# Performance work log

Hardware: AMD Instinct MI355X
Metric: run time of the kernel (lower is better)

The kernel has to match this reference:

```python
import jax, jax.numpy as jnp
import numpy as np

B, IN, E, H, V, MAX_LEN = 512, 64, 512, 1024, 1024, 32
LN_EPS = 1e-5


def setup_inputs() -> dict:
    key = jax.random.key(0)
    ks = jax.random.split(key, 16)
    s = 0.02
    n = lambda k, shp: jax.random.normal(k, shp, jnp.float32) * s
    return {
        "x": jax.random.normal(ks[0], (B, IN), jnp.float32),
        "w_in": n(ks[1], (E, IN)), "b_in": jnp.zeros((E,), jnp.float32),
        "w_ih0": n(ks[2], (4 * H, E)), "w_hh0": n(ks[3], (4 * H, H)),
        "b_ih0": jnp.zeros((4 * H,), jnp.float32), "b_hh0": jnp.zeros((4 * H,), jnp.float32),
        "w_ih1": n(ks[4], (4 * H, H)), "w_hh1": n(ks[5], (4 * H, H)),
        "b_ih1": jnp.zeros((4 * H,), jnp.float32), "b_hh1": jnp.zeros((4 * H,), jnp.float32),
        "ln_g": jnp.ones((H,), jnp.float32), "ln_b": jnp.zeros((H,), jnp.float32),
        "w_out": n(ks[6], (V, H)), "b_out": jnp.zeros((V,), jnp.float32),
        "emb": n(ks[7], (V, E)),
    }


def _lstm_cell(x, h, c, w_ih, w_hh, b_ih, b_hh):
    # PyTorch LSTMCell: gates ordered (input, forget, cell, output)
    gates = x @ w_ih.T + h @ w_hh.T + b_ih + b_hh  # [B, 4H]
    i, f, g, o = jnp.split(gates, 4, axis=1)
    i, f, o = jax.nn.sigmoid(i), jax.nn.sigmoid(f), jax.nn.sigmoid(o)
    g = jnp.tanh(g)
    c2 = f * c + i * g
    h2 = o * jnp.tanh(c2)
    return h2, c2


def reference(x, w_in, b_in, w_ih0, w_hh0, b_ih0, b_hh0,
              w_ih1, w_hh1, b_ih1, b_hh1, ln_g, ln_b, w_out, b_out, emb):
    bsz = x.shape[0]
    hid = w_hh0.shape[1]
    inp = x @ w_in.T + b_in  # [B, E]
    z = jnp.zeros((bsz, hid), jnp.float32)
    init = (z, z, z, z, inp)

    def step(carry, _):
        h0, c0, h1, c1, cur = carry
        h0, c0 = _lstm_cell(cur, h0, c0, w_ih0, w_hh0, b_ih0, b_hh0)
        h1, c1 = _lstm_cell(h0, h1, c1, w_ih1, w_hh1, b_ih1, b_hh1)
        mu = jnp.mean(h1, axis=-1, keepdims=True)
        var = jnp.mean((h1 - mu) ** 2, axis=-1, keepdims=True)
        hn = (h1 - mu) / jnp.sqrt(var + LN_EPS) * ln_g + ln_b
        lp = jax.nn.log_softmax(hn @ w_out.T + b_out, axis=-1)  # [B, V]
        ent = -jnp.sum(jnp.exp(lp) * lp, axis=-1)  # [B]
        sym = jnp.argmax(lp, axis=-1)  # eval-mode (deterministic) path
        logprob = jnp.take_along_axis(lp, sym[:, None], axis=1)[:, 0]
        nxt = emb[sym]  # [B, E]
        return (h0, c0, h1, c1, nxt), (sym, logprob, ent)

    _, (seq, logits, ent) = jax.lax.scan(step, init, None, length=MAX_LEN)
    seq, logits, ent = seq.T, logits.T, ent.T  # [B, MAX_LEN]
    zcol_f = jnp.zeros((bsz, 1), jnp.float32)
    zcol_i = jnp.zeros((bsz, 1), seq.dtype)
    seq = jnp.concatenate([seq, zcol_i], axis=1)
    logits = jnp.concatenate([logits, zcol_f], axis=1)
    ent = jnp.concatenate([ent, zcol_f], axis=1)
    return seq, logits, ent
```

## Files before the change

### kernel.cpp

```cpp
#include <hip/hip_runtime.h>
#include <hip/hip_bf16.h>
#include <math.h>

#define BQ   512
#define EDIM 512
#define HDIM 1024
#define VDIM 1024
#define TLEN 32
#define TOUT 33
#define PGS  (BQ * 4 * HDIM)
#define PLS  (BQ * VDIM)

typedef _Float16 half8  __attribute__((ext_vector_type(8)));
typedef _Float16 half4v __attribute__((ext_vector_type(4)));
typedef float    f32x16 __attribute__((ext_vector_type(16)));

#define GLOAD_LDS16(gp, lp) __builtin_amdgcn_global_load_lds( \
    (const __attribute__((address_space(1))) void*)(gp),      \
    (__attribute__((address_space(3))) void*)(lp), 16, 0, 0)

__device__ __forceinline__ size_t packoff(int r, int k, int K) {
    return (size_t)(r >> 5) * (size_t)(32 * K) + (size_t)(k >> 4) * 512
         + (size_t)((k >> 3) & 1) * 256 + (size_t)(r & 31) * 8 + (size_t)(k & 7);
}

__device__ _Float16 g_curh[BQ*EDIM], g_curl[BQ*EDIM];
__device__ _Float16 g_h0h[BQ*HDIM], g_h0l[BQ*HDIM];
__device__ _Float16 g_h1h[BQ*HDIM], g_h1l[BQ*HDIM];
__device__ _Float16 g_hnh[BQ*HDIM], g_hnl[BQ*HDIM];
__device__ float    g_c0[BQ*HDIM], g_c1[BQ*HDIM];

__device__ _Float16 g_wih0h[4*HDIM*EDIM], g_wih0l[4*HDIM*EDIM];
__device__ _Float16 g_whh0h[4*HDIM*HDIM], g_whh0l[4*HDIM*HDIM];
__device__ _Float16 g_wih1h[4*HDIM*HDIM], g_wih1l[4*HDIM*HDIM];
__device__ _Float16 g_whh1h[4*HDIM*HDIM], g_whh1l[4*HDIM*HDIM];
__device__ _Float16 g_wouth[VDIM*HDIM],   g_woutl[VDIM*HDIM];

__device__ float g_part_g[4 * PGS];
__device__ float g_part_lg[8 * PLS];
__device__ float g_bsum0[4*HDIM], g_bsum1[4*HDIM];

__global__ void init_kernel(float* __restrict__ out,
                            const float* __restrict__ bi0, const float* __restrict__ bh0,
                            const float* __restrict__ bi1, const float* __restrict__ bh1) {
    int i = blockIdx.x * 256 + threadIdx.x;
    g_c0[i] = 0.f; g_c1[i] = 0.f;
    g_h0h[i] = (_Float16)0.f; g_h0l[i] = (_Float16)0.f;
    g_h1h[i] = (_Float16)0.f; g_h1l[i] = (_Float16)0.f;
    if (i < 4 * HDIM) {
        g_bsum0[i] = bi0[i] + bh0[i];
        g_bsum1[i] = bi1[i] + bh1[i];
    }
    if (i < 3 * BQ) {
        int which = i / BQ, b = i % BQ;
        out[(size_t)which * BQ * TOUT + (size_t)b * TOUT + (TOUT - 1)] = 0.f;
    }
}

__global__ void split_pack_kernel(const float* __restrict__ w, _Float16* __restrict__ hi,
                                  _Float16* __restrict__ lo, int klog, int nquads) {
    int q = blockIdx.x * 256 + threadIdx.x;
    if (q >= nquads) return;
    int e = q * 4;
    int r = e >> klog, k = e & ((1 << klog) - 1);
    float4 v = ((const float4*)w)[q];
    half4v h, l;
    h[0] = (_Float16)v.x; l[0] = (_Float16)((v.x - (float)h[0]) * 4096.f);
    h[1] = (_Float16)v.y; l[1] = (_Float16)((v.y - (float)h[1]) * 4096.f);
    h[2] = (_Float16)v.z; l[2] = (_Float16)((v.z - (float)h[2]) * 4096.f);
    h[3] = (_Float16)v.w; l[3] = (_Float16)((v.w - (float)h[3]) * 4096.f);
    size_t po = packoff(r, k, 1 << klog);
    *(half4v*)&hi[po] = h;
    *(half4v*)&lo[po] = l;
}

__device__ __forceinline__ void split1(float x, _Float16* hp, _Float16* lp) {
    _Float16 h = (_Float16)x;
    *hp = h;
    *lp = (_Float16)((x - (float)h) * 4096.f);
}

__global__ __launch_bounds__(256, 2) void gemm_rb(
    const _Float16* __restrict__ Ah1, const _Float16* __restrict__ Al1, int K1,
    const _Float16* __restrict__ Wh1, const _Float16* __restrict__ Wl1,
    const _Float16* __restrict__ Ah2, const _Float16* __restrict__ Al2, int K2,
    const _Float16* __restrict__ Wh2, const _Float16* __restrict__ Wl2,
    float* __restrict__ outp, int N, int S, int NTP)
{
    __shared__ __align__(16) _Float16 sA[4][2][4][512];
    __shared__ __align__(16) _Float16 sB[4][2][4][512];
    int tid = threadIdx.x;
    int l = tid & 63, w = tid >> 6;
    int lr = l & 31, lq = l >> 5;
    int mw = w >> 1, nw = w & 1;

    int wb = blockIdx.x;
    int xcd = wb & 7, q = wb >> 3;
    int nt = xcd * NTP + q % NTP;
    int rest = q / NTP;
    int s = rest % S;
    int mb = rest / S;

    int kch1 = K1 / S, kch2 = (K2 > 0) ? (K2 / S) : 0;
    int n1 = kch1 >> 4;
    int nit = n1 + (kch2 >> 4);

    const _Float16* fsrc1[4];
    const _Float16* fsrc2[4];
    _Float16* fdst0[4];
    #pragma unroll
    for (int qq = 0; qq < 4; ++qq) {
        int fq = w * 4 + qq;
        bool isA = fq < 8;
        int r_ = isA ? fq : fq - 8;
        int pl = r_ >> 2, idx = r_ & 3;
        int strip = isA ? (mb * 4 + idx) : (nt * 4 + idx);
        const _Float16* p1 = isA ? (pl ? Al1 : Ah1) : (pl ? Wl1 : Wh1);
        fsrc1[qq] = p1 + (size_t)strip * (size_t)(32 * K1)
                  + (size_t)((s * kch1) >> 4) * 512 + (size_t)l * 8;
        if (K2 > 0) {
            const _Float16* p2 = isA ? (pl ? Al2 : Ah2) : (pl ? Wl2 : Wh2);
            fsrc2[qq] = p2 + (size_t)strip * (size_t)(32 * K2)
                      + (size_t)((s * kch2) >> 4) * 512 + (size_t)l * 8;
        } else {
            fsrc2[qq] = fsrc1[qq];
        }
        fdst0[qq] = isA ? &sA[0][pl][idx][0] : &sB[0][pl][idx][0];
    }

    f32x16 accM00 = {}, accM01 = {}, accM10 = {}, accM11 = {};
    f32x16 accL00 = {}, accL01 = {}, accL10 = {}, accL11 = {};

#define STAGE(IT, SLOT)                                                        \
    {                                                                          \
        int it_ = (IT);                                                        \
        bool g1_ = it_ < n1;                                                   \
        size_t off_ = (size_t)(g1_ ? it_ : it_ - n1) * 512;                    \
        _Pragma("unroll")                                                      \
        for (int qq = 0; qq < 4; ++qq) {                                       \
            const _Float16* sp_ = (g1_ ? fsrc1[qq] : fsrc2[qq]) + off_;        \
            GLOAD_LDS16(sp_, fdst0[qq] + (size_t)(SLOT) * 4096);               \
        }                                                                      \
    }

#define COMPUTE(BUF)                                                           \
    {                                                                          \
        half8 ah0 = *(const half8*)&sA[BUF][0][2*mw  ][(size_t)l * 8];         \
        half8 ah1 = *(const half8*)&sA[BUF][0][2*mw+1][(size_t)l * 8];         \
        half8 al0 = *(const half8*)&sA[BUF][1][2*mw  ][(size_t)l * 8];         \
        half8 al1 = *(const half8*)&sA[BUF][1][2*mw+1][(size_t)l * 8];         \
        half8 bh0 = *(const half8*)&sB[BUF][0][2*nw  ][(size_t)l * 8];         \
        half8 bh1 = *(const half8*)&sB[BUF][0][2*nw+1][(size_t)l * 8];         \
        half8 bl0 = *(const half8*)&sB[BUF][1][2*nw  ][(size_t)l * 8];         \
        half8 bl1 = *(const half8*)&sB[BUF][1][2*nw+1][(size_t)l * 8];         \
        accM00 = __builtin_amdgcn_mfma_f32_32x32x16_f16(ah0, bh0, accM00, 0, 0, 0); \
        accM01 = __builtin_amdgcn_mfma_f32_32x32x16_f16(ah0, bh1, accM01, 0, 0, 0); \
        accM10 = __builtin_amdgcn_mfma_f32_32x32x16_f16(ah1, bh0, accM10, 0, 0, 0); \
        accM11 = __builtin_amdgcn_mfma_f32_32x32x16_f16(ah1, bh1, accM11, 0, 0, 0); \
        accL00 = __builtin_amdgcn_mfma_f32_32x32x16_f16(ah0, bl0, accL00, 0, 0, 0); \
        accL01 = __builtin_amdgcn_mfma_f32_32x32x16_f16(ah0, bl1, accL01, 0, 0, 0); \
        accL10 = __builtin_amdgcn_mfma_f32_32x32x16_f16(ah1, bl0, accL10, 0, 0, 0); \
        accL11 = __builtin_amdgcn_mfma_f32_32x32x16_f16(ah1, bl1, accL11, 0, 0, 0); \
        accL00 = __builtin_amdgcn_mfma_f32_32x32x16_f16(al0, bh0, accL00, 0, 0, 0); \
        accL01 = __builtin_amdgcn_mfma_f32_32x32x16_f16(al0, bh1, accL01, 0, 0, 0); \
        accL10 = __builtin_amdgcn_mfma_f32_32x32x16_f16(al1, bh0, accL10, 0, 0, 0); \
        accL11 = __builtin_amdgcn_mfma_f32_32x32x16_f16(al1, bh1, accL11, 0, 0, 0); \
    }

#define WAITSYNC(IT)                                                           \
    {                                                                          \
        if ((IT) < nit - 2)       asm volatile("s_waitcnt vmcnt(8)" ::: "memory"); \
        else if ((IT) == nit - 2) asm volatile("s_waitcnt vmcnt(4)" ::: "memory"); \
        else                      asm volatile("s_waitcnt vmcnt(0)" ::: "memory"); \
        __builtin_amdgcn_sched_barrier(0);                                     \
        __builtin_amdgcn_s_barrier();                                          \
    }

    STAGE(0, 0);
    STAGE(1, 1);
    for (int it = 0; it < nit; ++it) {
        if (it + 2 < nit) STAGE(it + 2, (it + 2) & 3);
        WAITSYNC(it);
        COMPUTE(it & 3);
    }
#undef WAITSYNC
#undef COMPUTE
#undef STAGE

    float* op = outp + (size_t)s * BQ * N;
    #pragma unroll
    for (int mi = 0; mi < 2; ++mi) {
        int m0 = mb * 128 + (mw * 2 + mi) * 32;
        #pragma unroll
        for (int ni = 0; ni < 2; ++ni) {
            int n = nt * 128 + (nw * 2 + ni) * 32 + lr;
            const f32x16* aM = (mi == 0) ? (ni == 0 ? &accM00 : &accM01)
                                         : (ni == 0 ? &accM10 : &accM11);
            const f32x16* aL = (mi == 0) ? (ni == 0 ? &accL00 : &accL01)
                                         : (ni == 0 ? &accL10 : &accL11);
            #pragma unroll
            for (int r = 0; r < 16; ++r) {
                int row = (r & 3) + 8 * (r >> 2) + 4 * lq;
                op[(size_t)(m0 + row) * N + n] = (*aM)[r] + (*aL)[r] * (1.f / 4096.f);
            }
        }
    }
}

#define GBK 16
#define GPAD 68
__global__ __launch_bounds__(256) void gemm_in(const float* __restrict__ x,
                                               const float* __restrict__ w_in,
                                               const float* __restrict__ b_in) {
    __shared__ __align__(16) float As[GBK][GPAD];
    __shared__ __align__(16) float Bs[GBK][GPAD];
    int tid = threadIdx.x;
    int tx = tid & 15, ty = tid >> 4;
    int m0 = blockIdx.y * 64, n0 = blockIdx.x * 64;
    int lm = tid >> 2, lk = (tid & 3) << 2;
    const int K = 64;
    float acc[4][4] = {};
    for (int k0 = 0; k0 < K; k0 += GBK) {
        float4 av = *(const float4*)(x + (size_t)(m0 + lm) * K + k0 + lk);
        float4 wv = *(const float4*)(w_in + (size_t)(n0 + lm) * K + k0 + lk);
        As[lk + 0][lm] = av.x; As[lk + 1][lm] = av.y;
        As[lk + 2][lm] = av.z; As[lk + 3][lm] = av.w;
        Bs[lk + 0][lm] = wv.x; Bs[lk + 1][lm] = wv.y;
        Bs[lk + 2][lm] = wv.z; Bs[lk + 3][lm] = wv.w;
        __syncthreads();
        #pragma unroll
        for (int kk = 0; kk < GBK; ++kk) {
            float4 a  = *(const float4*)&As[kk][ty * 4];
            float4 bq = *(const float4*)&Bs[kk][tx * 4];
            float aa[4] = {a.x, a.y, a.z, a.w};
            float bb[4] = {bq.x, bq.y, bq.z, bq.w};
            #pragma unroll
            for (int i = 0; i < 4; ++i)
                #pragma unroll
                for (int j = 0; j < 4; ++j)
                    acc[i][j] = fmaf(aa[i], bb[j], acc[i][j]);
        }
        __syncthreads();
    }
    #pragma unroll
    for (int i = 0; i < 4; ++i) {
        int m = m0 + ty * 4 + i;
        int n = n0 + tx * 4;
        half4v h, lo;
        #pragma unroll
        for (int j = 0; j < 4; ++j) {
            float v = acc[i][j] + b_in[n + j];
            _Float16 hv = (_Float16)v;
            h[j] = hv;
            lo[j] = (_Float16)((v - (float)hv) * 4096.f);
        }
        size_t po = packoff(m, n, EDIM);
        *(half4v*)&g_curh[po] = h;
        *(half4v*)&g_curl[po] = lo;
    }
}

__device__ __forceinline__ float sigm(float x) { return 1.f / (1.f + expf(-x)); }

__global__ void lstm0_kernel() {
    int qidx = blockIdx.x * 256 + threadIdx.x;
    int b = qidx >> 8;
    int j = (qidx & 255) * 4;
    size_t base = (size_t)b * 4096;
    float4 G[4];
    #pragma unroll
    for (int g = 0; g < 4; ++g) {
        float4 bs = *(const float4*)&g_bsum0[g * 1024 + j];
        G[g] = bs;
        #pragma unroll
        for (int s = 0; s < 4; ++s) {
            float4 p = *(const float4*)&g_part_g[(size_t)s * PGS + base + g * 1024 + j];
            G[g].x += p.x; G[g].y += p.y; G[g].z += p.z; G[g].w += p.w;
        }
    }
    size_t hb = (size_t)b * HDIM + j;
    float4 cin = *(const float4*)&g_c0[hb];
    float ci[4] = {cin.x, cin.y, cin.z, cin.w};
    float gi[4] = {G[0].x, G[0].y, G[0].z, G[0].w};
    float gf[4] = {G[1].x, G[1].y, G[1].z, G[1].w};
    float gg[4] = {G[2].x, G[2].y, G[2].z, G[2].w};
    float go[4] = {G[3].x, G[3].y, G[3].z, G[3].w};
    float c[4], h[4];
    half4v hh, hl;
    #pragma unroll
    for (int r = 0; r < 4; ++r) {
        c[r] = sigm(gf[r]) * ci[r] + sigm(gi[r]) * tanhf(gg[r]);
        h[r] = sigm(go[r]) * tanhf(c[r]);
        _Float16 hi16 = (_Float16)h[r];
        hh[r] = hi16;
        hl[r] = (_Float16)((h[r] - (float)hi16) * 4096.f);
    }
    *(float4*)&g_c0[hb] = {c[0], c[1], c[2], c[3]};
    size_t po = packoff(b, j, HDIM);
    *(half4v*)&g_h0h[po] = hh;
    *(half4v*)&g_h0l[po] = hl;
}

__global__ __launch_bounds__(256) void lstm1_ln_kernel(
    const float* __restrict__ ln_g, const float* __restrict__ ln_b)
{
    __shared__ float sbuf[4];
    int b = blockIdx.x, tid = threadIdx.x;
    int lane = tid & 63, wid = tid >> 6;
    int j = tid * 4;
    size_t base = (size_t)b * 4096;
    float4 G[4];
    #pragma unroll
    for (int g = 0; g < 4; ++g) {
        float4 bs = *(const float4*)&g_bsum1[g * 1024 + j];
        G[g] = bs;
        #pragma unroll
        for (int s = 0; s < 4; ++s) {
            float4 p = *(const float4*)&g_part_g[(size_t)s * PGS + base + g * 1024 + j];
            G[g].x += p.x; G[g].y += p.y; G[g].z += p.z; G[g].w += p.w;
        }
    }
    size_t hb = (size_t)b * HDIM + j;
    float4 cin = *(const float4*)&g_c1[hb];
    float ci[4] = {cin.x, cin.y, cin.z, cin.w};
    float gi[4] = {G[0].x, G[0].y, G[0].z, G[0].w};
    float gf[4] = {G[1].x, G[1].y, G[1].z, G[1].w};
    float gg[4] = {G[2].x, G[2].y, G[2].z, G[2].w};
    float go[4] = {G[3].x, G[3].y, G[3].z, G[3].w};
    float c[4], h[4];
    float sum = 0.f;
    #pragma unroll
    for (int r = 0; r < 4; ++r) {
        c[r] = sigm(gf[r]) * ci[r] + sigm(gi[r]) * tanhf(gg[r]);
        h[r] = sigm(go[r]) * tanhf(c[r]);
        sum += h[r];
    }
    *(float4*)&g_c1[hb] = {c[0], c[1], c[2], c[3]};
    size_t po = packoff(b, j, HDIM);
    half4v h1h, h1l;
    #pragma unroll
    for (int r = 0; r < 4; ++r) {
        _Float16 hi16 = (_Float16)h[r];
        h1h[r] = hi16;
        h1l[r] = (_Float16)((h[r] - (float)hi16) * 4096.f);
    }
    *(half4v*)&g_h1h[po] = h1h;
    *(half4v*)&g_h1l[po] = h1l;

    for (int off = 32; off > 0; off >>= 1) sum += __shfl_down(sum, off, 64);
    if (lane == 0) sbuf[wid] = sum;
    __syncthreads();
    float mu = (sbuf[0] + sbuf[1] + sbuf[2] + sbuf[3]) * (1.f / HDIM);
    __syncthreads();
    float sq = 0.f;
    #pragma unroll
    for (int r = 0; r < 4; ++r) { float d = h[r] - mu; sq += d * d; }
    for (int off = 32; off > 0; off >>= 1) sq += __shfl_down(sq, off, 64);
    if (lane == 0) sbuf[wid] = sq;
    __syncthreads();
    float var = (sbuf[0] + sbuf[1] + sbuf[2] + sbuf[3]) * (1.f / HDIM);
    float rstd = 1.f / sqrtf(var + 1e-5f);
    half4v nh, nl;
    #pragma unroll
    for (int r = 0; r < 4; ++r) {
        float hn = (h[r] - mu) * rstd * ln_g[j + r] + ln_b[j + r];
        _Float16 hi16 = (_Float16)hn;
        nh[r] = hi16;
        nl[r] = (_Float16)((hn - (float)hi16) * 4096.f);
    }
    *(half4v*)&g_hnh[po] = nh;
    *(half4v*)&g_hnl[po] = nl;
}

__global__ __launch_bounds__(256) void softmax_row_kernel(
    const float* __restrict__ b_out, const float* __restrict__ emb,
    float* __restrict__ out, int t)
{
    __shared__ float swv[4];
    __shared__ int   swi[4];
    __shared__ float sZ[4], sS[4];
    __shared__ float s_max;
    __shared__ int   s_idx;
    int b = blockIdx.x, tid = threadIdx.x;
    int lane = tid & 63, wid = tid >> 6;
    size_t base = (size_t)b * VDIM + 4 * tid;
    float4 xv = *(const float4*)&b_out[4 * tid];
    #pragma unroll
    for (int s = 0; s < 8; ++s) {
        float4 p = *(const float4*)&g_part_lg[(size_t)s * PLS + base];
        xv.x += p.x; xv.y += p.y; xv.z += p.z; xv.w += p.w;
    }

    float mv = xv.x; int mi = 4 * tid;
    if (xv.y > mv) { mv = xv.y; mi = 4 * tid + 1; }
    if (xv.z > mv) { mv = xv.z; mi = 4 * tid + 2; }
    if (xv.w > mv) { mv = xv.w; mi = 4 * tid + 3; }
    for (int off = 32; off > 0; off >>= 1) {
        float ov = __shfl_down(mv, off, 64);
        int   oi = __shfl_down(mi, off, 64);
        if (ov > mv || (ov == mv && oi < mi)) { mv = ov; mi = oi; }
    }
    if (lane == 0) { swv[wid] = mv; swi[wid] = mi; }
    __syncthreads();
    if (tid == 0) {
        mv = swv[0]; mi = swi[0];
        for (int w = 1; w < 4; ++w)
            if (swv[w] > mv || (swv[w] == mv && swi[w] < mi)) { mv = swv[w]; mi = swi[w]; }
        s_max = mv; s_idx = mi;
    }
    __syncthreads();
    float xmax = s_max;

    float sv[4] = {xv.x - xmax, xv.y - xmax, xv.z - xmax, xv.w - xmax};
    float z = 0.f, s1 = 0.f;
    #pragma unroll
    for (int r = 0; r < 4; ++r) { float e = expf(sv[r]); z += e; s1 += e * sv[r]; }
    for (int off = 32; off > 0; off >>= 1) {
        z  += __shfl_down(z, off, 64);
        s1 += __shfl_down(s1, off, 64);
    }
    if (lane == 0) { sZ[wid] = z; sS[wid] = s1; }
    __syncthreads();
    if (tid == 0) {
        float Z = sZ[0] + sZ[1] + sZ[2] + sZ[3];
        float S1 = sS[0] + sS[1] + sS[2] + sS[3];
        float logZ = logf(Z);
        float ent = logZ - S1 / Z;
        out[(size_t)b * TOUT + t]                         = (float)s_idx;
        out[(size_t)BQ * TOUT + (size_t)b * TOUT + t]     = -logZ;
        out[(size_t)2 * BQ * TOUT + (size_t)b * TOUT + t] = ent;
    }
    __syncthreads();
    int sym = s_idx;
    const float* e = emb + (size_t)sym * EDIM;
    for (int j = tid; j < EDIM; j += 256) {
        size_t po = packoff(b, j, EDIM);
        split1(e[j], &g_curh[po], &g_curl[po]);
    }
}

extern "C" void kernel_launch(void* const* d_in, const int* in_sizes, int n_in,
                              void* d_out, int out_size, void* d_ws, size_t ws_size,
                              hipStream_t stream) {
    const float* x     = (const float*)d_in[0];
    const float* w_in  = (const float*)d_in[1];
    const float* b_in  = (const float*)d_in[2];
    const float* w_ih0 = (const float*)d_in[3];
    const float* w_hh0 = (const float*)d_in[4];
    const float* b_ih0 = (const float*)d_in[5];
    const float* b_hh0 = (const float*)d_in[6];
    const float* w_ih1 = (const float*)d_in[7];
    const float* w_hh1 = (const float*)d_in[8];
    const float* b_ih1 = (const float*)d_in[9];
    const float* b_hh1 = (const float*)d_in[10];
    const float* ln_g  = (const float*)d_in[11];
    const float* ln_b  = (const float*)d_in[12];
    const float* w_out = (const float*)d_in[13];
    const float* b_out = (const float*)d_in[14];
    const float* emb   = (const float*)d_in[15];
    float* out = (float*)d_out;

    _Float16 *wih0h, *wih0l, *whh0h, *whh0l, *wih1h, *wih1l, *whh1h, *whh1l, *wouth, *woutl;
    hipGetSymbolAddress((void**)&wih0h, HIP_SYMBOL(g_wih0h));
    hipGetSymbolAddress((void**)&wih0l, HIP_SYMBOL(g_wih0l));
    hipGetSymbolAddress((void**)&whh0h, HIP_SYMBOL(g_whh0h));
    hipGetSymbolAddress((void**)&whh0l, HIP_SYMBOL(g_whh0l));
    hipGetSymbolAddress((void**)&wih1h, HIP_SYMBOL(g_wih1h));
    hipGetSymbolAddress((void**)&wih1l, HIP_SYMBOL(g_wih1l));
    hipGetSymbolAddress((void**)&whh1h, HIP_SYMBOL(g_whh1h));
    hipGetSymbolAddress((void**)&whh1l, HIP_SYMBOL(g_whh1l));
    hipGetSymbolAddress((void**)&wouth, HIP_SYMBOL(g_wouth));
    hipGetSymbolAddress((void**)&woutl, HIP_SYMBOL(g_woutl));
    _Float16 *curh, *curl, *h0h, *h0l, *h1h, *h1l, *hnh, *hnl;
    hipGetSymbolAddress((void**)&curh, HIP_SYMBOL(g_curh));
    hipGetSymbolAddress((void**)&curl, HIP_SYMBOL(g_curl));
    hipGetSymbolAddress((void**)&h0h, HIP_SYMBOL(g_h0h));
    hipGetSymbolAddress((void**)&h0l, HIP_SYMBOL(g_h0l));
    hipGetSymbolAddress((void**)&h1h, HIP_SYMBOL(g_h1h));
    hipGetSymbolAddress((void**)&h1l, HIP_SYMBOL(g_h1l));
    hipGetSymbolAddress((void**)&hnh, HIP_SYMBOL(g_hnh));
    hipGetSymbolAddress((void**)&hnl, HIP_SYMBOL(g_hnl));
    float *part_g, *part_lg;
    hipGetSymbolAddress((void**)&part_g, HIP_SYMBOL(g_part_g));
    hipGetSymbolAddress((void**)&part_lg, HIP_SYMBOL(g_part_lg));

    init_kernel<<<(BQ * HDIM) / 256, 256, 0, stream>>>(out, b_ih0, b_hh0, b_ih1, b_hh1);

    split_pack_kernel<<<(4*HDIM*EDIM/4 + 255)/256, 256, 0, stream>>>(w_ih0, wih0h, wih0l, 9,  4*HDIM*EDIM/4);
    split_pack_kernel<<<(4*HDIM*HDIM/4 + 255)/256, 256, 0, stream>>>(w_hh0, whh0h, whh0l, 10, 4*HDIM*HDIM/4);
    split_pack_kernel<<<(4*HDIM*HDIM/4 + 255)/256, 256, 0, stream>>>(w_ih1, wih1h, wih1l, 10, 4*HDIM*HDIM/4);
    split_pack_kernel<<<(4*HDIM*HDIM/4 + 255)/256, 256, 0, stream>>>(w_hh1, whh1h, whh1l, 10, 4*HDIM*HDIM/4);
    split_pack_kernel<<<(VDIM*HDIM/4 + 255)/256, 256, 0, stream>>>(w_out, wouth, woutl, 10, VDIM*HDIM/4);

    gemm_in<<<dim3(EDIM / 64, BQ / 64), 256, 0, stream>>>(x, w_in, b_in);

    for (int t = 0; t < TLEN; ++t) {
        gemm_rb<<<512, 256, 0, stream>>>(
            curh, curl, EDIM, wih0h, wih0l,
            h0h, h0l, HDIM, whh0h, whh0l,
            part_g, 4 * HDIM, 4, 4);
        lstm0_kernel<<<(BQ * HDIM / 4) / 256, 256, 0, stream>>>();

        gemm_rb<<<512, 256, 0, stream>>>(
            h0h, h0l, HDIM, wih1h, wih1l,
            h1h, h1l, HDIM, whh1h, whh1l,
            part_g, 4 * HDIM, 4, 4);
        lstm1_ln_kernel<<<BQ, 256, 0, stream>>>(ln_g, ln_b);

        gemm_rb<<<256, 256, 0, stream>>>(
            hnh, hnl, HDIM, wouth, woutl,
            (const _Float16*)nullptr, (const _Float16*)nullptr, 0,
            (const _Float16*)nullptr, (const _Float16*)nullptr,
            part_lg, VDIM, 8, 1);

        softmax_row_kernel<<<BQ, 256, 0, stream>>>(b_out, emb, out, t);
    }
}
```

Before: 2.968 ms.

## Load B weight fragments directly into registers instead of staging through LDS

The GEMM now stages only the A operand through shared memory with global_load_lds and loads each wave's B (weight) fragments straight from global memory into registers, double-buffered across two register sets with the loop unrolled by two. The aim is to halve LDS traffic and footprint, since each B fragment is used by only one wave pair. It also wraps the MFMA chain in s_setprio. The vmcnt accounting is adjusted, but the loop assumes an even iteration count and adds register pressure, with possible uncoalesced or exposed global latency on B.

```diff
diff --git a/kernel.cpp b/kernel.cpp
--- a/kernel.cpp
+++ b/kernel.cpp
@@ -88,7 +88,6 @@
     float* __restrict__ outp, int N, int S, int NTP)
 {
     __shared__ __align__(16) _Float16 sA[4][2][4][512];
-    __shared__ __align__(16) _Float16 sB[4][2][4][512];
     int tid = threadIdx.x;
     int l = tid & 63, w = tid >> 6;
     int lr = l & 31, lq = l >> 5;
@@ -105,87 +104,122 @@
     int n1 = kch1 >> 4;
     int nit = n1 + (kch2 >> 4);
 
-    const _Float16* fsrc1[4];
-    const _Float16* fsrc2[4];
-    _Float16* fdst0[4];
-    #pragma unroll
-    for (int qq = 0; qq < 4; ++qq) {
-        int fq = w * 4 + qq;
-        bool isA = fq < 8;
-        int r_ = isA ? fq : fq - 8;
-        int pl = r_ >> 2, idx = r_ & 3;
-        int strip = isA ? (mb * 4 + idx) : (nt * 4 + idx);
-        const _Float16* p1 = isA ? (pl ? Al1 : Ah1) : (pl ? Wl1 : Wh1);
-        fsrc1[qq] = p1 + (size_t)strip * (size_t)(32 * K1)
-                  + (size_t)((s * kch1) >> 4) * 512 + (size_t)l * 8;
+    const _Float16* fsrcA1[2];
+    const _Float16* fsrcA2[2];
+    _Float16* fdstA[2];
+    #pragma unroll
+    for (int qq = 0; qq < 2; ++qq) {
+        int f = w * 2 + qq;
+        int pl = f >> 2, mf = f & 3;
+        const _Float16* p1 = pl ? Al1 : Ah1;
+        fsrcA1[qq] = p1 + (size_t)(mb * 4 + mf) * (size_t)(32 * K1)
+                   + (size_t)((s * kch1) >> 4) * 512 + (size_t)l * 8;
         if (K2 > 0) {
-            const _Float16* p2 = isA ? (pl ? Al2 : Ah2) : (pl ? Wl2 : Wh2);
-            fsrc2[qq] = p2 + (size_t)strip * (size_t)(32 * K2)
-                      + (size_t)((s * kch2) >> 4) * 512 + (size_t)l * 8;
+            const _Float16* p2 = pl ? Al2 : Ah2;
+            fsrcA2[qq] = p2 + (size_t)(mb * 4 + mf) * (size_t)(32 * K2)
+                       + (size_t)((s * kch2) >> 4) * 512 + (size_t)l * 8;
         } else {
-            fsrc2[qq] = fsrc1[qq];
-        }
-        fdst0[qq] = isA ? &sA[0][pl][idx][0] : &sB[0][pl][idx][0];
+            fsrcA2[qq] = fsrcA1[qq];
+        }
+        fdstA[qq] = &sA[0][pl][mf][0];
+    }
+
+    const _Float16 *pB1[4], *pB2[4];
+    #pragma unroll
+    for (int pj = 0; pj < 4; ++pj) {
+        int pl = pj >> 1, j = pj & 1;
+        const _Float16* p1 = pl ? Wl1 : Wh1;
+        pB1[pj] = p1 + (size_t)(nt * 4 + 2 * nw + j) * (size_t)(32 * K1)
+                + (size_t)((s * kch1) >> 4) * 512 + (size_t)l * 8;
+        if (K2 > 0) {
+            const _Float16* p2 = pl ? Wl2 : Wh2;
+            pB2[pj] = p2 + (size_t)(nt * 4 + 2 * nw + j) * (size_t)(32 * K2)
+                    + (size_t)((s * kch2) >> 4) * 512 + (size_t)l * 8;
+        } else {
+            pB2[pj] = pB1[pj];
+        }
     }
 
     f32x16 accM00 = {}, accM01 = {}, accM10 = {}, accM11 = {};
     f32x16 accL00 = {}, accL01 = {}, accL10 = {}, accL11 = {};
 
-#define STAGE(IT, SLOT)                                                        \
+    half8 B0h0, B0h1, B0l0, B0l1;
+    half8 B1h0, B1h1, B1l0, B1l1;
+
+#define STAGE_A(IT, SLOT)                                                      \
     {                                                                          \
         int it_ = (IT);                                                        \
         bool g1_ = it_ < n1;                                                   \
         size_t off_ = (size_t)(g1_ ? it_ : it_ - n1) * 512;                    \
         _Pragma("unroll")                                                      \
-        for (int qq = 0; qq < 4; ++qq) {                                       \
-            const _Float16* sp_ = (g1_ ? fsrc1[qq] : fsrc2[qq]) + off_;        \
-            GLOAD_LDS16(sp_, fdst0[qq] + (size_t)(SLOT) * 4096);               \
+        for (int qq = 0; qq < 2; ++qq) {                                       \
+            const _Float16* sp_ = (g1_ ? fsrcA1[qq] : fsrcA2[qq]) + off_;      \
+            GLOAD_LDS16(sp_, fdstA[qq] + (size_t)(SLOT) * 4096);               \
         }                                                                      \
     }
 
-#define COMPUTE(BUF)                                                           \
+#define LOAD_B(IT, BH0, BH1, BL0, BL1)                                         \
     {                                                                          \
-        half8 ah0 = *(const half8*)&sA[BUF][0][2*mw  ][(size_t)l * 8];         \
-        half8 ah1 = *(const half8*)&sA[BUF][0][2*mw+1][(size_t)l * 8];         \
-        half8 al0 = *(const half8*)&sA[BUF][1][2*mw  ][(size_t)l * 8];         \
-        half8 al1 = *(const half8*)&sA[BUF][1][2*mw+1][(size_t)l * 8];         \
-        half8 bh0 = *(const half8*)&sB[BUF][0][2*nw  ][(size_t)l * 8];         \
-        half8 bh1 = *(const half8*)&sB[BUF][0][2*nw+1][(size_t)l * 8];         \
-        half8 bl0 = *(const half8*)&sB[BUF][1][2*nw  ][(size_t)l * 8];         \
-        half8 bl1 = *(const half8*)&sB[BUF][1][2*nw+1][(size_t)l * 8];         \
-        accM00 = __builtin_amdgcn_mfma_f32_32x32x16_f16(ah0, bh0, accM00, 0, 0, 0); \
-        accM01 = __builtin_amdgcn_mfma_f32_32x32x16_f16(ah0, bh1, accM01, 0, 0, 0); \
-        accM10 = __builtin_amdgcn_mfma_f32_32x32x16_f16(ah1, bh0, accM10, 0, 0, 0); \
-        accM11 = __builtin_amdgcn_mfma_f32_32x32x16_f16(ah1, bh1, accM11, 0, 0, 0); \
-        accL00 = __builtin_amdgcn_mfma_f32_32x32x16_f16(ah0, bl0, accL00, 0, 0, 0); \
-        accL01 = __builtin_amdgcn_mfma_f32_32x32x16_f16(ah0, bl1, accL01, 0, 0, 0); \
-        accL10 = __builtin_amdgcn_mfma_f32_32x32x16_f16(ah1, bl0, accL10, 0, 0, 0); \
-        accL11 = __builtin_amdgcn_mfma_f32_32x32x16_f16(ah1, bl1, accL11, 0, 0, 0); \
-        accL00 = __builtin_amdgcn_mfma_f32_32x32x16_f16(al0, bh0, accL00, 0, 0, 0); \
-        accL01 = __builtin_amdgcn_mfma_f32_32x32x16_f16(al0, bh1, accL01, 0, 0, 0); \
-        accL10 = __builtin_amdgcn_mfma_f32_32x32x16_f16(al1, bh0, accL10, 0, 0, 0); \
-        accL11 = __builtin_amdgcn_mfma_f32_32x32x16_f16(al1, bh1, accL11, 0, 0, 0); \
+        int it_ = (IT);                                                        \
+        bool g1_ = it_ < n1;                                                   \
+        size_t off_ = (size_t)(g1_ ? it_ : it_ - n1) * 512;                    \
+        BH0 = *(const half8*)((g1_ ? pB1[0] : pB2[0]) + off_);                 \
+        BH1 = *(const half8*)((g1_ ? pB1[1] : pB2[1]) + off_);                 \
+        BL0 = *(const half8*)((g1_ ? pB1[2] : pB2[2]) + off_);                 \
+        BL1 = *(const half8*)((g1_ ? pB1[3] : pB2[3]) + off_);                 \
+    }
+
+#define COMPUTE(SLOT, BH0, BH1, BL0, BL1)                                      \
+    {                                                                          \
+        half8 ah0 = *(const half8*)&sA[SLOT][0][2*mw  ][(size_t)l * 8];        \
+        half8 ah1 = *(const half8*)&sA[SLOT][0][2*mw+1][(size_t)l * 8];        \
+        half8 al0 = *(const half8*)&sA[SLOT][1][2*mw  ][(size_t)l * 8];        \
+        half8 al1 = *(const half8*)&sA[SLOT][1][2*mw+1][(size_t)l * 8];        \
+        __builtin_amdgcn_s_setprio(1);                                         \
+        accM00 = __builtin_amdgcn_mfma_f32_32x32x16_f16(ah0, BH0, accM00, 0, 0, 0); \
+        accM01 = __builtin_amdgcn_mfma_f32_32x32x16_f16(ah0, BH1, accM01, 0, 0, 0); \
+        accM10 = __builtin_amdgcn_mfma_f32_32x32x16_f16(ah1, BH0, accM10, 0, 0, 0); \
+        accM11 = __builtin_amdgcn_mfma_f32_32x32x16_f16(ah1, BH1, accM11, 0, 0, 0); \
+        accL00 = __builtin_amdgcn_mfma_f32_32x32x16_f16(ah0, BL0, accL00, 0, 0, 0); \
+        accL01 = __builtin_amdgcn_mfma_f32_32x32x16_f16(ah0, BL1, accL01, 0, 0, 0); \
+        accL10 = __builtin_amdgcn_mfma_f32_32x32x16_f16(ah1, BL0, accL10, 0, 0, 0); \
+        accL11 = __builtin_amdgcn_mfma_f32_32x32x16_f16(ah1, BL1, accL11, 0, 0, 0); \
+        accL00 = __builtin_amdgcn_mfma_f32_32x32x16_f16(al0, BH0, accL00, 0, 0, 0); \
+        accL01 = __builtin_amdgcn_mfma_f32_32x32x16_f16(al0, BH1, accL01, 0, 0, 0); \
+        accL10 = __builtin_amdgcn_mfma_f32_32x32x16_f16(al1, BH0, accL10, 0, 0, 0); \
+        accL11 = __builtin_amdgcn_mfma_f32_32x32x16_f16(al1, BH1, accL11, 0, 0, 0); \
+        __builtin_amdgcn_s_setprio(0);                                         \
     }
 
 #define WAITSYNC(IT)                                                           \
     {                                                                          \
-        if ((IT) < nit - 2)       asm volatile("s_waitcnt vmcnt(8)" ::: "memory"); \
-        else if ((IT) == nit - 2) asm volatile("s_waitcnt vmcnt(4)" ::: "memory"); \
-        else                      asm volatile("s_waitcnt vmcnt(0)" ::: "memory"); \
+        int rem_ = nit - 1 - (IT);                                             \
+        if (rem_ >= 2)      asm volatile("s_waitcnt vmcnt(8)" ::: "memory");   \
+        else if (rem_ == 1) asm volatile("s_waitcnt vmcnt(6)" ::: "memory");   \
+        else                asm volatile("s_waitcnt vmcnt(0)" ::: "memory");   \
         __builtin_amdgcn_sched_barrier(0);                                     \
         __builtin_amdgcn_s_barrier();                                          \
     }
 
-    STAGE(0, 0);
-    STAGE(1, 1);
-    for (int it = 0; it < nit; ++it) {
-        if (it + 2 < nit) STAGE(it + 2, (it + 2) & 3);
+    STAGE_A(0, 0);
+    LOAD_B(0, B0h0, B0h1, B0l0, B0l1);
+    STAGE_A(1, 1);
+
+    for (int it = 0; it < nit; it += 2) {
+        if (it + 1 < nit) LOAD_B(it + 1, B1h0, B1h1, B1l0, B1l1);
+        if (it + 2 < nit) STAGE_A(it + 2, (it + 2) & 3);
         WAITSYNC(it);
-        COMPUTE(it & 3);
+        COMPUTE(it & 3, B0h0, B0h1, B0l0, B0l1);
+
+        if (it + 2 < nit) LOAD_B(it + 2, B0h0, B0h1, B0l0, B0l1);
+        if (it + 3 < nit) STAGE_A(it + 3, (it + 3) & 3);
+        WAITSYNC(it + 1);
+        COMPUTE((it + 1) & 3, B1h0, B1h1, B1l0, B1l1);
     }
 #undef WAITSYNC
 #undef COMPUTE
-#undef STAGE
+#undef LOAD_B
+#undef STAGE_A
 
     float* op = outp + (size_t)s * BQ * N;
     #pragma unroll
```

Result: slower. 3.127 ms (+5.4%).

## Double K-step per iteration with two-slot LDS buffering and MFMA priority

Applied to the files above, without the earlier changes.

Each main-loop iteration of the split-fp16 GEMM now loads and computes a 32-wide K chunk instead of 16. The four-slot ring with prefetch depth two becomes a two-slot double buffer with prefetch depth one, which halves the number of barriers and waitcnt points per K. MFMA blocks are wrapped in s_setprio so compute waves are favoured over loads. Total LDS use is unchanged. The risk is a hazard: a fast wave can start the async load into the slot that slower waves are still reading from the previous iteration. The change also assumes each split K chunk is a multiple of 32.

```diff
diff --git a/kernel.cpp b/kernel.cpp
--- a/kernel.cpp
+++ b/kernel.cpp
@@ -87,8 +87,8 @@
     const _Float16* __restrict__ Wh2, const _Float16* __restrict__ Wl2,
     float* __restrict__ outp, int N, int S, int NTP)
 {
-    __shared__ __align__(16) _Float16 sA[4][2][4][512];
-    __shared__ __align__(16) _Float16 sB[4][2][4][512];
+    __shared__ __align__(16) _Float16 sA[2][2][4][2][512];
+    __shared__ __align__(16) _Float16 sB[2][2][4][2][512];
     int tid = threadIdx.x;
     int l = tid & 63, w = tid >> 6;
     int lr = l & 31, lq = l >> 5;
@@ -102,30 +102,30 @@
     int mb = rest / S;
 
     int kch1 = K1 / S, kch2 = (K2 > 0) ? (K2 / S) : 0;
-    int n1 = kch1 >> 4;
-    int nit = n1 + (kch2 >> 4);
-
-    const _Float16* fsrc1[4];
-    const _Float16* fsrc2[4];
-    _Float16* fdst0[4];
-    #pragma unroll
-    for (int qq = 0; qq < 4; ++qq) {
-        int fq = w * 4 + qq;
-        bool isA = fq < 8;
-        int r_ = isA ? fq : fq - 8;
-        int pl = r_ >> 2, idx = r_ & 3;
+    int n1 = kch1 >> 5;
+    int nit = n1 + (kch2 >> 5);
+
+    const _Float16* fsrc1[8];
+    const _Float16* fsrc2[8];
+    _Float16* fdst0[8];
+    #pragma unroll
+    for (int qq = 0; qq < 8; ++qq) {
+        int f = w * 8 + qq;
+        bool isA = f < 16;
+        int r_ = isA ? f : f - 16;
+        int pl = r_ >> 3, idx = (r_ >> 1) & 3, kh = r_ & 1;
         int strip = isA ? (mb * 4 + idx) : (nt * 4 + idx);
         const _Float16* p1 = isA ? (pl ? Al1 : Ah1) : (pl ? Wl1 : Wh1);
         fsrc1[qq] = p1 + (size_t)strip * (size_t)(32 * K1)
-                  + (size_t)((s * kch1) >> 4) * 512 + (size_t)l * 8;
+                  + (size_t)((s * kch1) >> 4) * 512 + (size_t)kh * 512 + (size_t)l * 8;
         if (K2 > 0) {
             const _Float16* p2 = isA ? (pl ? Al2 : Ah2) : (pl ? Wl2 : Wh2);
             fsrc2[qq] = p2 + (size_t)strip * (size_t)(32 * K2)
-                      + (size_t)((s * kch2) >> 4) * 512 + (size_t)l * 8;
+                      + (size_t)((s * kch2) >> 4) * 512 + (size_t)kh * 512 + (size_t)l * 8;
         } else {
             fsrc2[qq] = fsrc1[qq];
         }
-        fdst0[qq] = isA ? &sA[0][pl][idx][0] : &sB[0][pl][idx][0];
+        fdst0[qq] = isA ? &sA[0][pl][idx][kh][0] : &sB[0][pl][idx][kh][0];
     }
 
     f32x16 accM00 = {}, accM01 = {}, accM10 = {}, accM11 = {};
@@ -135,24 +135,25 @@
     {                                                                          \
         int it_ = (IT);                                                        \
         bool g1_ = it_ < n1;                                                   \
-        size_t off_ = (size_t)(g1_ ? it_ : it_ - n1) * 512;                    \
+        size_t off_ = (size_t)(g1_ ? it_ : it_ - n1) * 1024;                   \
         _Pragma("unroll")                                                      \
-        for (int qq = 0; qq < 4; ++qq) {                                       \
+        for (int qq = 0; qq < 8; ++qq) {                                       \
             const _Float16* sp_ = (g1_ ? fsrc1[qq] : fsrc2[qq]) + off_;        \
-            GLOAD_LDS16(sp_, fdst0[qq] + (size_t)(SLOT) * 4096);               \
+            GLOAD_LDS16(sp_, fdst0[qq] + (size_t)(SLOT) * 8192);               \
         }                                                                      \
     }
 
-#define COMPUTE(BUF)                                                           \
+#define COMPUTE(SLOT, KH)                                                      \
     {                                                                          \
-        half8 ah0 = *(const half8*)&sA[BUF][0][2*mw  ][(size_t)l * 8];         \
-        half8 ah1 = *(const half8*)&sA[BUF][0][2*mw+1][(size_t)l * 8];         \
-        half8 al0 = *(const half8*)&sA[BUF][1][2*mw  ][(size_t)l * 8];         \
-        half8 al1 = *(const half8*)&sA[BUF][1][2*mw+1][(size_t)l * 8];         \
-        half8 bh0 = *(const half8*)&sB[BUF][0][2*nw  ][(size_t)l * 8];         \
-        half8 bh1 = *(const half8*)&sB[BUF][0][2*nw+1][(size_t)l * 8];         \
-        half8 bl0 = *(const half8*)&sB[BUF][1][2*nw  ][(size_t)l * 8];         \
-        half8 bl1 = *(const half8*)&sB[BUF][1][2*nw+1][(size_t)l * 8];         \
+        half8 ah0 = *(const half8*)&sA[SLOT][0][2*mw  ][KH][(size_t)l * 8];    \
+        half8 ah1 = *(const half8*)&sA[SLOT][0][2*mw+1][KH][(size_t)l * 8];    \
+        half8 al0 = *(const half8*)&sA[SLOT][1][2*mw  ][KH][(size_t)l * 8];    \
+        half8 al1 = *(const half8*)&sA[SLOT][1][2*mw+1][KH][(size_t)l * 8];    \
+        half8 bh0 = *(const half8*)&sB[SLOT][0][2*nw  ][KH][(size_t)l * 8];    \
+        half8 bh1 = *(const half8*)&sB[SLOT][0][2*nw+1][KH][(size_t)l * 8];    \
+        half8 bl0 = *(const half8*)&sB[SLOT][1][2*nw  ][KH][(size_t)l * 8];    \
+        half8 bl1 = *(const half8*)&sB[SLOT][1][2*nw+1][KH][(size_t)l * 8];    \
+        __builtin_amdgcn_s_setprio(1);                                         \
         accM00 = __builtin_amdgcn_mfma_f32_32x32x16_f16(ah0, bh0, accM00, 0, 0, 0); \
         accM01 = __builtin_amdgcn_mfma_f32_32x32x16_f16(ah0, bh1, accM01, 0, 0, 0); \
         accM10 = __builtin_amdgcn_mfma_f32_32x32x16_f16(ah1, bh0, accM10, 0, 0, 0); \
@@ -165,25 +166,22 @@
         accL01 = __builtin_amdgcn_mfma_f32_32x32x16_f16(al0, bh1, accL01, 0, 0, 0); \
         accL10 = __builtin_amdgcn_mfma_f32_32x32x16_f16(al1, bh0, accL10, 0, 0, 0); \
         accL11 = __builtin_amdgcn_mfma_f32_32x32x16_f16(al1, bh1, accL11, 0, 0, 0); \
-    }
-
-#define WAITSYNC(IT)                                                           \
-    {                                                                          \
-        if ((IT) < nit - 2)       asm volatile("s_waitcnt vmcnt(8)" ::: "memory"); \
-        else if ((IT) == nit - 2) asm volatile("s_waitcnt vmcnt(4)" ::: "memory"); \
-        else                      asm volatile("s_waitcnt vmcnt(0)" ::: "memory"); \
-        __builtin_amdgcn_sched_barrier(0);                                     \
-        __builtin_amdgcn_s_barrier();                                          \
+        __builtin_amdgcn_s_setprio(0);                                         \
     }
 
     STAGE(0, 0);
-    STAGE(1, 1);
     for (int it = 0; it < nit; ++it) {
-        if (it + 2 < nit) STAGE(it + 2, (it + 2) & 3);
-        WAITSYNC(it);
-        COMPUTE(it & 3);
-    }
-#undef WAITSYNC
+        if (it + 1 < nit) {
+            STAGE(it + 1, (it + 1) & 1);
+            asm volatile("s_waitcnt vmcnt(8)" ::: "memory");
+        } else {
+            asm volatile("s_waitcnt vmcnt(0)" ::: "memory");
+        }
+        __builtin_amdgcn_sched_barrier(0);
+        __builtin_amdgcn_s_barrier();
+        COMPUTE(it & 1, 0);
+        COMPUTE(it & 1, 1);
+    }
 #undef COMPUTE
 #undef STAGE
 
```

Result: no change. 2.994 ms (+0.9%).
